# Kernel tuning notes

Hardware: AMD Instinct MI355X
Metric: run time of the kernel (lower is better)

Reference implementation:

```python
import jax, jax.numpy as jnp
import numpy as np

SEQ_LEN = 4096      # config.seq_len (num_blocks=1 so PosPerBlock == seq_len)
EMB = 3             # config.filter_emb_dim
FILTER_ORDER = 16   # config.filter_order
CH = 768            # HeadSizeOrderMinus1 = hidden_dim/num_heads*(order-1)
BATCH = 16
SHIFT = 0.0
MODULATE = True
USE_BIAS = True
FAST_DECAY_PCT = 0.3
SLOW_DECAY_PCT = 1.5
TARGET = 0.01


def _pos_emb(L):
    # PositionalEmbedding: t in [0,1], complex exponential bands
    t = jnp.linspace(0.0, 1.0, L)                      # [L]
    bands = (EMB - 1) // 2                              # = 1
    t_rescaled = jnp.linspace(0.0, float(L - 1), L)     # [L]
    w = 2.0 * jnp.pi * t_rescaled / L                   # [L]
    f = jnp.linspace(1e-4, float(max(bands - 1, 0)), bands)  # [bands]
    z_c = jnp.exp(-1j * f[None, :] * w[:, None])        # [L, bands]
    z = jnp.concatenate([t[:, None], jnp.real(z_c), jnp.imag(z_c)], axis=-1)  # [L, EMB]
    return z.astype(jnp.float32), t.astype(jnp.float32)


def _implicit_filter(L, w1, b1, w2, b2, w3, b3, freq, deltas_abs):
    z, t = _pos_emb(L)
    # MLP with trainable Sin activation (freq shared across layers)
    h = jnp.sin(freq * (z @ w1.T + b1))                 # [L, FILTER_ORDER]
    h = jnp.sin(freq * (h @ w2.T + b2))                 # [L, FILTER_ORDER]
    h = h @ w3.T + b3                                   # [L, CH]
    if MODULATE:
        decay = jnp.exp(-t[:, None] * deltas_abs[None, :])  # [L, CH]
        h = h * (decay + SHIFT)
    return h


def fft_conv(u, k):
    seqlen = u.shape[-2]
    fft_size = 2 * seqlen
    u_f = jnp.fft.rfft(u.astype(jnp.float32), n=fft_size, axis=-2)
    k_f = jnp.fft.rfft(k.astype(jnp.float32), n=fft_size, axis=-2) / fft_size
    y = jnp.fft.irfft(u_f * k_f, n=fft_size, axis=-2)[..., :seqlen, :]
    return y.astype(u.dtype)


def setup_inputs() -> dict:
    key = jax.random.key(0)
    ks = jax.random.split(key, 8)
    u = jax.random.normal(ks[0], (BATCH, SEQ_LEN, CH), dtype=jnp.float32)
    w1 = jax.random.normal(ks[1], (FILTER_ORDER, EMB), dtype=jnp.float32) * 0.5
    b1 = jax.random.normal(ks[2], (FILTER_ORDER,), dtype=jnp.float32) * 0.1
    w2 = jax.random.normal(ks[3], (FILTER_ORDER, FILTER_ORDER), dtype=jnp.float32) * 0.25
    b2 = jax.random.normal(ks[4], (FILTER_ORDER,), dtype=jnp.float32) * 0.1
    w3 = jax.random.normal(ks[5], (CH, FILTER_ORDER), dtype=jnp.float32) * 0.25
    b3 = jax.random.normal(ks[6], (CH,), dtype=jnp.float32) * 0.1
    freq = jnp.ones((FILTER_ORDER,), dtype=jnp.float32)  # Sin.init with w=1
    # ExponentialModulation.init
    max_decay = np.log(TARGET) / FAST_DECAY_PCT
    min_decay = np.log(TARGET) / SLOW_DECAY_PCT
    deltas_abs = jnp.abs(jnp.linspace(min_decay, max_decay, CH)).astype(jnp.float32)
    bias = jax.random.normal(ks[7], (CH,), dtype=jnp.float32)
    return {"u": u, "w1": w1, "b1": b1, "w2": w2, "b2": b2,
            "w3": w3, "b3": b3, "freq": freq, "deltas_abs": deltas_abs, "bias": bias}


def reference(u, w1, b1, w2, b2, w3, b3, freq, deltas_abs, bias):
    L = u.shape[-2]
    k = _implicit_filter(L, w1, b1, w2, b2, w3, b3, freq, deltas_abs)  # [L, CH]
    y = fft_conv(u, k)
    if USE_BIAS:
        y = y + u * bias  # bias broadcast over [B, L, CH]
    return y
```

## Files before the change

kernel.cpp:

```cpp
#include <hip/hip_runtime.h>
#include <hip/hip_bf16.h>

#define SEQ   4096
#define NFFT  8192
#define NCH   768
#define NB    16
#define KST   4104
#define LDSN  4368

typedef float cf __attribute__((ext_vector_type(2)));

__device__ __forceinline__ int phys(int p) { return p + (p >> 4) + (p >> 8); }
__device__ __forceinline__ int br12(int k) { return (int)(__brev((unsigned)k) >> 20); }

constexpr int BR4[16] = {0,8,4,12,2,10,6,14,1,9,5,13,3,11,7,15};

__device__ __forceinline__ cf cmul_wi(cf a, cf w, cf iw) {
  cf axx = __builtin_shufflevector(a, a, 0, 0);
  cf ayy = __builtin_shufflevector(a, a, 1, 1);
  return axx * w + ayy * iw;
}
__device__ __forceinline__ cf icmul(cf a) { return cf{-a.y, a.x}; }
__device__ __forceinline__ cf cmul(cf a, cf b) { return cmul_wi(a, b, icmul(b)); }

#define CMULC(a, WX, WY) cmul_wi(a, cf{(WX),(WY)}, cf{-(WY),(WX)})

#define C1X 0.9238795325112867f
#define C1Y (-0.3826834323650898f)
#define C2X 0.7071067811865476f
#define C2Y (-0.7071067811865476f)
#define C3X 0.3826834323650898f
#define C3Y (-0.9238795325112867f)

#define BF_F(a, b, WX, WY) { cf t_ = a - b; a = a + b; b = CMULC(t_, WX, WY); }
#define BF_F1(a, b)        { cf t_ = a - b; a = a + b; b = t_; }
#define BF_FJ(a, b)        { cf t_ = a - b; a = a + b; b = cf{t_.y, -t_.x}; }
#define BF_I(a, b, WX, WY) { cf t_ = cmul_wi(b, cf{(WX),-(WY)}, cf{(WY),(WX)}); b = a - t_; a = a + t_; }
#define BF_I1(a, b)        { cf t_ = b; b = a - t_; a = a + t_; }
#define BF_IJ(a, b)        { cf t_ = cf{-b.y, b.x}; b = a - t_; a = a + t_; }

__device__ __forceinline__ void dft16_f_tail(cf v[16]) {
  BF_F1(v[0], v[4]);            BF_F(v[1], v[5],  C2X, C2Y);
  BF_FJ(v[2], v[6]);            BF_F(v[3], v[7], -C2X, C2Y);
  BF_F1(v[8], v[12]);           BF_F(v[9], v[13], C2X, C2Y);
  BF_FJ(v[10], v[14]);          BF_F(v[11], v[15], -C2X, C2Y);
  BF_F1(v[0], v[2]);  BF_FJ(v[1], v[3]);
  BF_F1(v[4], v[6]);  BF_FJ(v[5], v[7]);
  BF_F1(v[8], v[10]); BF_FJ(v[9], v[11]);
  BF_F1(v[12], v[14]); BF_FJ(v[13], v[15]);
  BF_F1(v[0], v[1]);  BF_F1(v[2], v[3]);
  BF_F1(v[4], v[5]);  BF_F1(v[6], v[7]);
  BF_F1(v[8], v[9]);  BF_F1(v[10], v[11]);
  BF_F1(v[12], v[13]); BF_F1(v[14], v[15]);
}

__device__ __forceinline__ void dft16_f(cf v[16]) {
  BF_F1(v[0], v[8]);
  BF_F(v[1], v[9],  C1X, C1Y);
  BF_F(v[2], v[10], C2X, C2Y);
  BF_F(v[3], v[11], C3X, C3Y);
  BF_FJ(v[4], v[12]);
  BF_F(v[5], v[13], -C3X, C3Y);
  BF_F(v[6], v[14], -C2X, C2Y);
  BF_F(v[7], v[15], -C1X, C1Y);
  dft16_f_tail(v);
}

__device__ __forceinline__ void dft16_i(cf v[16]) {
  BF_I1(v[0], v[1]);  BF_I1(v[2], v[3]);
  BF_I1(v[4], v[5]);  BF_I1(v[6], v[7]);
  BF_I1(v[8], v[9]);  BF_I1(v[10], v[11]);
  BF_I1(v[12], v[13]); BF_I1(v[14], v[15]);
  BF_I1(v[0], v[2]);  BF_IJ(v[1], v[3]);
  BF_I1(v[4], v[6]);  BF_IJ(v[5], v[7]);
  BF_I1(v[8], v[10]); BF_IJ(v[9], v[11]);
  BF_I1(v[12], v[14]); BF_IJ(v[13], v[15]);
  BF_I1(v[0], v[4]);            BF_I(v[1], v[5],  C2X, C2Y);
  BF_IJ(v[2], v[6]);            BF_I(v[3], v[7], -C2X, C2Y);
  BF_I1(v[8], v[12]);           BF_I(v[9], v[13], C2X, C2Y);
  BF_IJ(v[10], v[14]);          BF_I(v[11], v[15], -C2X, C2Y);
  BF_I1(v[0], v[8]);
  BF_I(v[1], v[9],  C1X, C1Y);
  BF_I(v[2], v[10], C2X, C2Y);
  BF_I(v[3], v[11], C3X, C3Y);
  BF_IJ(v[4], v[12]);
  BF_I(v[5], v[13], -C3X, C3Y);
  BF_I(v[6], v[14], -C2X, C2Y);
  BF_I(v[7], v[15], -C1X, C1Y);
}

__device__ __forceinline__ void twiddle_apply(cf v[16], cf w1) {
  cf iw1 = icmul(w1);
  cf wr = w1, iwr = iw1;
  #pragma unroll
  for (int r = 1; r < 16; ++r) {
    v[BR4[r]] = cmul_wi(v[BR4[r]], wr, iwr);
    if (r < 15) { wr = cmul_wi(wr, w1, iw1); iwr = icmul(wr); }
  }
}

__device__ __forceinline__ void twiddle_f(cf v[16], int i, float invNP) {
  float sn, cs; __sincosf(-6.283185307179586f * (float)i * invNP, &sn, &cs);
  twiddle_apply(v, cf{cs, sn});
}
__device__ __forceinline__ void twiddle_i(cf v[16], int i, float invNP) {
  float sn, cs; __sincosf(6.283185307179586f * (float)i * invNP, &sn, &cs);
  twiddle_apply(v, cf{cs, sn});
}

__device__ __forceinline__ void pass_f_first(cf* X, int tid) {
  cf v[16];
  #pragma unroll
  for (int m = 0; m < 8; ++m) v[m] = X[phys(tid + m * 256)];
  v[8]  = v[0];
  v[9]  = CMULC(v[1],  C1X, C1Y);
  v[10] = CMULC(v[2],  C2X, C2Y);
  v[11] = CMULC(v[3],  C3X, C3Y);
  v[12] = cf{v[4].y, -v[4].x};
  v[13] = CMULC(v[5], -C3X, C3Y);
  v[14] = CMULC(v[6], -C2X, C2Y);
  v[15] = CMULC(v[7], -C1X, C1Y);
  dft16_f_tail(v);
  if (tid) twiddle_f(v, tid, 1.0f / 4096.0f);
  #pragma unroll
  for (int s = 0; s < 16; ++s) X[phys(tid + s * 256)] = v[s];
}

template<int NP>
__device__ __forceinline__ void pass_f(cf* X, int tid) {
  constexpr int G = NP / 16;
  int i = tid & (G - 1);
  int base = (tid & ~(G - 1)) * 16 + i;
  cf v[16];
  #pragma unroll
  for (int m = 0; m < 16; ++m) v[m] = X[phys(base + m * G)];
  dft16_f(v);
  if (G > 1 && i) twiddle_f(v, i, 1.0f / (float)NP);
  #pragma unroll
  for (int s = 0; s < 16; ++s) X[phys(base + s * G)] = v[s];
}

template<int NP>
__device__ __forceinline__ void pass_i(cf* X, int tid) {
  constexpr int G = NP / 16;
  int i = tid & (G - 1);
  int base = (tid & ~(G - 1)) * 16 + i;
  cf v[16];
  #pragma unroll
  for (int s = 0; s < 16; ++s) v[s] = X[phys(base + s * G)];
  if (G > 1 && i) twiddle_i(v, i, 1.0f / (float)NP);
  dft16_i(v);
  #pragma unroll
  for (int m = 0; m < 16; ++m) X[phys(base + m * G)] = v[m];
}

__device__ __forceinline__ void fft_forward(cf* X, int tid) {
  pass_f_first(X, tid); __syncthreads();
  pass_f<256>(X, tid);  __syncthreads();
  pass_f<16>(X, tid);   __syncthreads();
}
__device__ __forceinline__ void fft_inverse(cf* X, int tid) {
  pass_i<16>(X, tid);   __syncthreads();
  pass_i<256>(X, tid);  __syncthreads();
  pass_i<4096>(X, tid);
}

__device__ __forceinline__ void unpack_pair(cf Zk, cf Zq, float c_, float s_,
                                            cf& Xk, cf& Xm) {
  float Ex = 0.5f*(Zk.x + Zq.x), Ey = 0.5f*(Zk.y - Zq.y);
  float Ox = 0.5f*(Zk.y + Zq.y), Oy = 0.5f*(Zq.x - Zk.x);
  Xk = cf{Ex + c_*Ox + s_*Oy,  Ey + c_*Oy - s_*Ox};
  Xm = cf{Ex - c_*Ox - s_*Oy, -Ey + c_*Oy - s_*Ox};
}

__device__ __forceinline__ cf bf16pair_to_cf(unsigned int v) {
  return cf{__uint_as_float(v << 16), __uint_as_float(v & 0xFFFF0000u)};
}
__device__ __forceinline__ unsigned int cf_to_bf16pair(cf z) {
  unsigned int a = __float_as_uint(z.x), b = __float_as_uint(z.y);
  a = (a + 0x7FFFu + ((a >> 16) & 1u)) >> 16;
  b = (b + 0x7FFFu + ((b >> 16) & 1u)) & 0xFFFF0000u;
  return a | b;
}

__device__ __forceinline__ float mlp_eval(int n, const float* sw1, const float* sb1,
    const float* sw2, const float* sb2, const float* sfq, const float* sw3,
    float B3, float D) {
  float t = (float)n * (1.0f / 4095.0f);
  float fw = 1e-4f * 6.283185307179586f * (float)n / 4096.0f;
  float sfw, cfw; __sincosf(fw, &sfw, &cfw);
  float z0 = t, z1 = cfw, z2 = -sfw;
  float h1[16], h2[16];
  #pragma unroll
  for (int r = 0; r < 16; ++r)
    h1[r] = __sinf(sfq[r] * (z0 * sw1[3*r] + z1 * sw1[3*r+1] + z2 * sw1[3*r+2] + sb1[r]));
  #pragma unroll
  for (int r = 0; r < 16; ++r) {
    float acc = sb2[r];
    #pragma unroll
    for (int s = 0; s < 16; ++s) acc += h1[s] * sw2[16*r + s];
    h2[r] = __sinf(sfq[r] * acc);
  }
  float k = B3;
  #pragma unroll
  for (int r = 0; r < 16; ++r) k += h2[r] * sw3[r];
  return k * __expf(-t * D);
}

__global__ __launch_bounds__(256) void filter_fft_kernel(
    const float* __restrict__ w1, const float* __restrict__ b1,
    const float* __restrict__ w2, const float* __restrict__ b2,
    const float* __restrict__ w3, const float* __restrict__ b3,
    const float* __restrict__ freq, const float* __restrict__ deltas,
    cf* __restrict__ Kf) {
  __shared__ cf X[LDSN];
  __shared__ float sw1[48], sb1[16], sw2[256], sb2[16], sfq[16], sw3[16];
  int tid = threadIdx.x;
  int c = blockIdx.x;
  if (tid < 48) sw1[tid] = w1[tid];
  if (tid < 16) { sb1[tid] = b1[tid]; sb2[tid] = b2[tid]; sfq[tid] = freq[tid];
                  sw3[tid] = w3[(size_t)c * 16 + tid]; }
  sw2[tid] = w2[tid];
  float B3 = b3[c], D = deltas[c];
  __syncthreads();

  #pragma unroll
  for (int j = 0; j < 8; ++j) {
    int n2 = tid + 256 * j;
    float k0 = mlp_eval(2*n2,     sw1, sb1, sw2, sb2, sfq, sw3, B3, D);
    float k1 = mlp_eval(2*n2 + 1, sw1, sb1, sw2, sb2, sfq, sw3, B3, D);
    X[phys(n2)] = cf{k0, k1};
  }

  fft_forward(X, tid);

  const float SC = 1.0f / 33554432.0f;
  cf* Kc = Kf + (size_t)c * KST;
  for (int k = tid; k <= 2048; k += 256) {
    int kq = (4096 - k) & 4095;
    cf Zk = X[phys(br12(k))], Zq = X[phys(br12(kq))];
    float c_, s_; __sincosf((float)k * (3.14159265358979e0f / 4096.0f), &s_, &c_);
    cf Xk, Xm;
    unpack_pair(Zk, Zq, c_, s_, Xk, Xm);
    Kc[k]        = SC * Xk;
    Kc[4096 - k] = SC * Xm;
  }
}

__global__ __launch_bounds__(256) void transpose_in(
    const float* __restrict__ u, __hip_bfloat16* __restrict__ ut) {
  __shared__ float tile[64][65];
  int i0 = blockIdx.x * 64, c0 = blockIdx.y * 64, b = blockIdx.z;
  int tr = threadIdx.x >> 6, tc = threadIdx.x & 63;
  const float* up = u + ((size_t)b * SEQ + i0) * NCH + c0;
  for (int r = tr; r < 64; r += 4) tile[r][tc] = up[(size_t)r * NCH + tc];
  __syncthreads();
  __hip_bfloat16* op = ut + ((size_t)b * NCH + c0) * SEQ + i0;
  for (int r = tr; r < 64; r += 4) op[(size_t)r * SEQ + tc] = __float2bfloat16(tile[tc][r]);
}

__global__ __launch_bounds__(256) void conv_kernel(
    __hip_bfloat16* __restrict__ ut, const cf* __restrict__ Kf) {
  __shared__ cf X[LDSN];
  int tid = threadIdx.x;
  int wg  = blockIdx.x;
  int id  = (wg & 7) * (NCH * NB / 8) + (wg >> 3);
  int c   = id >> 4;
  int b   = id & 15;
  unsigned int* row = (unsigned int*)(ut + ((size_t)b * NCH + c) * SEQ);
  const cf* Kc = Kf + (size_t)c * KST;

  #pragma unroll
  for (int j = 0; j < 8; ++j) {
    int n2 = tid + 256 * j;
    X[phys(n2)] = bf16pair_to_cf(row[n2]);
  }

  fft_forward(X, tid);

  for (int k = tid; k <= 2048; k += 256) {
    int kq = (4096 - k) & 4095;
    int p = phys(br12(k));
    int q = phys(br12(kq));
    cf Zk = X[p], Zq = X[q];
    float c_, s_; __sincosf((float)k * (3.14159265358979e0f / 4096.0f), &s_, &c_);
    cf Xk, Xm;
    unpack_pair(Zk, Zq, c_, s_, Xk, Xm);
    cf Yk = cmul(Xk, Kc[k]);
    cf Ym = cmul(Xm, Kc[4096 - k]);
    float Ax = 0.5f*(Yk.x + Ym.x), Ay = 0.5f*(Yk.y - Ym.y);
    float Bx = 0.5f*(Yk.x - Ym.x), By = 0.5f*(Yk.y + Ym.y);
    X[p] = cf{Ax - c_*By - s_*Bx,  Ay + c_*Bx - s_*By};
    X[q] = cf{Ax + c_*By + s_*Bx, -Ay + c_*Bx - s_*By};
  }
  __syncthreads();

  fft_inverse(X, tid);

  #pragma unroll
  for (int j = 0; j < 8; ++j) {
    int n2 = tid + 256 * j;
    row[n2] = cf_to_bf16pair(X[phys(n2)]);
  }
}

__global__ __launch_bounds__(256) void transpose_out(
    const __hip_bfloat16* __restrict__ yt, const float* __restrict__ u,
    const float* __restrict__ bias, float* __restrict__ y) {
  __shared__ float tile[64][65];
  int i0 = blockIdx.x * 64, c0 = blockIdx.y * 64, b = blockIdx.z;
  int tr = threadIdx.x >> 6, tc = threadIdx.x & 63;
  const __hip_bfloat16* yp = yt + ((size_t)b * NCH + c0) * SEQ + i0;
  for (int r = tr; r < 64; r += 4) tile[r][tc] = __bfloat162float(yp[(size_t)r * SEQ + tc]);
  __syncthreads();
  float bi = bias[c0 + tc];
  const float* up = u + ((size_t)b * SEQ + i0) * NCH + c0;
  float* op = y + ((size_t)b * SEQ + i0) * NCH + c0;
  for (int r = tr; r < 64; r += 4)
    op[(size_t)r * NCH + tc] = tile[tc][r] + up[(size_t)r * NCH + tc] * bi;
}

extern "C" void kernel_launch(void* const* d_in, const int* in_sizes, int n_in,
                              void* d_out, int out_size, void* d_ws, size_t ws_size,
                              hipStream_t stream) {
  const float* u      = (const float*)d_in[0];
  const float* w1     = (const float*)d_in[1];
  const float* b1     = (const float*)d_in[2];
  const float* w2     = (const float*)d_in[3];
  const float* b2     = (const float*)d_in[4];
  const float* w3     = (const float*)d_in[5];
  const float* b3     = (const float*)d_in[6];
  const float* freq   = (const float*)d_in[7];
  const float* deltas = (const float*)d_in[8];
  const float* bias   = (const float*)d_in[9];
  float* out = (float*)d_out;

  __hip_bfloat16* ut = (__hip_bfloat16*)d_ws;
  cf* Kf = (cf*)((char*)d_ws + (size_t)NB * NCH * SEQ * 2);

  filter_fft_kernel<<<dim3(NCH), dim3(256), 0, stream>>>(w1, b1, w2, b2, w3, b3, freq, deltas, Kf);
  transpose_in<<<dim3(SEQ / 64, NCH / 64, NB), dim3(256), 0, stream>>>(u, ut);
  conv_kernel<<<dim3(NCH * NB), dim3(256), 0, stream>>>(ut, Kf);
  transpose_out<<<dim3(SEQ / 64, NCH / 64, NB), dim3(256), 0, stream>>>(ut, u, bias, out);
}
```

Measured before the change: 485.9 us.

## Fuse transposes and bias into FFT convolution kernel with strided direct access

Removes the separate transpose-in and transpose-out kernels and the bf16 intermediate buffer. The conv kernel now reads u directly with a channel-strided gather, keeps the inputs in registers, and writes y with the bias term added. The block-to-channel mapping groups neighbouring channels on the same XCD so that L2 can reuse cache lines. Each global access is an uncoalesced 4-byte strided access that relies on cache line sharing between concurrent blocks.

Result: slower. 636.1 us (+30.9%).

```diff
diff --git a/kernel.cpp b/kernel.cpp
--- a/kernel.cpp
+++ b/kernel.cpp
@@ -173,16 +173,6 @@
   Xm = cf{Ex - c_*Ox - s_*Oy, -Ey + c_*Oy - s_*Ox};
 }
 
-__device__ __forceinline__ cf bf16pair_to_cf(unsigned int v) {
-  return cf{__uint_as_float(v << 16), __uint_as_float(v & 0xFFFF0000u)};
-}
-__device__ __forceinline__ unsigned int cf_to_bf16pair(cf z) {
-  unsigned int a = __float_as_uint(z.x), b = __float_as_uint(z.y);
-  a = (a + 0x7FFFu + ((a >> 16) & 1u)) >> 16;
-  b = (b + 0x7FFFu + ((b >> 16) & 1u)) & 0xFFFF0000u;
-  return a | b;
-}
-
 __device__ __forceinline__ float mlp_eval(int n, const float* sw1, const float* sb1,
     const float* sw2, const float* sb2, const float* sfq, const float* sw3,
     float B3, float D) {
@@ -247,33 +237,34 @@
   }
 }
 
-__global__ __launch_bounds__(256) void transpose_in(
-    const float* __restrict__ u, __hip_bfloat16* __restrict__ ut) {
-  __shared__ float tile[64][65];
-  int i0 = blockIdx.x * 64, c0 = blockIdx.y * 64, b = blockIdx.z;
-  int tr = threadIdx.x >> 6, tc = threadIdx.x & 63;
-  const float* up = u + ((size_t)b * SEQ + i0) * NCH + c0;
-  for (int r = tr; r < 64; r += 4) tile[r][tc] = up[(size_t)r * NCH + tc];
-  __syncthreads();
-  __hip_bfloat16* op = ut + ((size_t)b * NCH + c0) * SEQ + i0;
-  for (int r = tr; r < 64; r += 4) op[(size_t)r * SEQ + tc] = __float2bfloat16(tile[tc][r]);
-}
-
-__global__ __launch_bounds__(256) void conv_kernel(
-    __hip_bfloat16* __restrict__ ut, const cf* __restrict__ Kf) {
+__global__ __launch_bounds__(256) void fused_conv(
+    const float* __restrict__ u, const cf* __restrict__ Kf,
+    const float* __restrict__ bias, float* __restrict__ y) {
   __shared__ cf X[LDSN];
   int tid = threadIdx.x;
   int wg  = blockIdx.x;
-  int id  = (wg & 7) * (NCH * NB / 8) + (wg >> 3);
-  int c   = id >> 4;
-  int b   = id & 15;
-  unsigned int* row = (unsigned int*)(ut + ((size_t)b * NCH + c) * SEQ);
+  int xcd = wg & 7;
+  int idx = wg >> 3;
+  int b   = idx / 96;
+  int cw  = idx - b * 96;
+  int c   = xcd * 96 + cw;
+
+  const float* up = u + (size_t)b * SEQ * NCH + c;
+  float*       yp = y + (size_t)b * SEQ * NCH + c;
   const cf* Kc = Kf + (size_t)c * KST;
-
+  float bi = bias[c];
+
+  float u0[8], u1[8];
   #pragma unroll
   for (int j = 0; j < 8; ++j) {
     int n2 = tid + 256 * j;
-    X[phys(n2)] = bf16pair_to_cf(row[n2]);
+    u0[j] = up[(size_t)(2 * n2) * NCH];
+    u1[j] = up[(size_t)(2 * n2 + 1) * NCH];
+  }
+  #pragma unroll
+  for (int j = 0; j < 8; ++j) {
+    int n2 = tid + 256 * j;
+    X[phys(n2)] = cf{u0[j], u1[j]};
   }
 
   fft_forward(X, tid);
@@ -300,24 +291,10 @@
   #pragma unroll
   for (int j = 0; j < 8; ++j) {
     int n2 = tid + 256 * j;
-    row[n2] = cf_to_bf16pair(X[phys(n2)]);
-  }
-}
-
-__global__ __launch_bounds__(256) void transpose_out(
-    const __hip_bfloat16* __restrict__ yt, const float* __restrict__ u,
-    const float* __restrict__ bias, float* __restrict__ y) {
-  __shared__ float tile[64][65];
-  int i0 = blockIdx.x * 64, c0 = blockIdx.y * 64, b = blockIdx.z;
-  int tr = threadIdx.x >> 6, tc = threadIdx.x & 63;
-  const __hip_bfloat16* yp = yt + ((size_t)b * NCH + c0) * SEQ + i0;
-  for (int r = tr; r < 64; r += 4) tile[r][tc] = __bfloat162float(yp[(size_t)r * SEQ + tc]);
-  __syncthreads();
-  float bi = bias[c0 + tc];
-  const float* up = u + ((size_t)b * SEQ + i0) * NCH + c0;
-  float* op = y + ((size_t)b * SEQ + i0) * NCH + c0;
-  for (int r = tr; r < 64; r += 4)
-    op[(size_t)r * NCH + tc] = tile[tc][r] + up[(size_t)r * NCH + tc] * bi;
+    cf z = X[phys(n2)];
+    yp[(size_t)(2 * n2) * NCH]     = z.x + u0[j] * bi;
+    yp[(size_t)(2 * n2 + 1) * NCH] = z.y + u1[j] * bi;
+  }
 }
 
 extern "C" void kernel_launch(void* const* d_in, const int* in_sizes, int n_in,
@@ -335,11 +312,8 @@
   const float* bias   = (const float*)d_in[9];
   float* out = (float*)d_out;
 
-  __hip_bfloat16* ut = (__hip_bfloat16*)d_ws;
-  cf* Kf = (cf*)((char*)d_ws + (size_t)NB * NCH * SEQ * 2);
+  cf* Kf = (cf*)d_ws;
 
   filter_fft_kernel<<<dim3(NCH), dim3(256), 0, stream>>>(w1, b1, w2, b2, w3, b3, freq, deltas, Kf);
-  transpose_in<<<dim3(SEQ / 64, NCH / 64, NB), dim3(256), 0, stream>>>(u, ut);
-  conv_kernel<<<dim3(NCH * NB), dim3(256), 0, stream>>>(ut, Kf);
-  transpose_out<<<dim3(SEQ / 64, NCH / 64, NB), dim3(256), 0, stream>>>(ut, u, bias, out);
-}
+  fused_conv<<<dim3(NCH * NB), dim3(256), 0, stream>>>(u, Kf, bias, out);
+}
```
